# Performance work log

Hardware: AMD Instinct MI355X
Metric: run time of the kernel (lower is better)

Reference implementation:

```python
import jax, jax.numpy as jnp
import numpy as np
import math

D_MODEL = 1024
N_HEADS = 16
D_HEAD = D_MODEL // N_HEADS  # 64
ROPE_BASE = 10000.0


def make_inv_freq(dim: int, base: float = ROPE_BASE) -> jnp.ndarray:
    half = dim // 2
    if half == 0:
        return jnp.zeros((1,), dtype=jnp.float32)
    return jnp.asarray(1.0 / base ** (np.arange(half, dtype=np.float32) * 2.0 / dim))


def rope_1d(x, pos, inv_freq):
    # x: (B, H, L, d_slice); pos: (B, 1, L)
    D = x.shape[-1]
    half = D // 2
    if half == 0:
        return x
    f = pos[..., None].astype(jnp.float32) * inv_freq  # (B,1,L,half)
    c, s = jnp.cos(f), jnp.sin(f)
    x1, x2 = x[..., :half], x[..., half:2 * half]
    out = jnp.concatenate([x1 * c - x2 * s, x2 * c + x1 * s], axis=-1)
    if D > 2 * half:
        out = jnp.concatenate([out, x[..., 2 * half:]], axis=-1)
    return out


def rope_3d(x, rows, cols, pairs):
    # x: (B, H, L, D_HEAD); rows/cols/pairs: (B, L)
    d_per = D_HEAD // 3
    d_row = D_HEAD - 2 * d_per  # 22
    d_col = d_per               # 21
    d1, d2 = d_row, d_row + d_col
    r = rows[:, None, :]
    c = cols[:, None, :]
    p = pairs[:, None, :]
    x_row = rope_1d(x[..., :d1], r, make_inv_freq(d_row))
    x_col = rope_1d(x[..., d1:d2], c, make_inv_freq(d_col))
    x_pair = rope_1d(x[..., d2:], p, make_inv_freq(d_per))
    return jnp.concatenate([x_row, x_col, x_pair], axis=-1)


def setup_inputs() -> dict:
    key = jax.random.key(0)
    ks = jax.random.split(key, 8)
    B, L, D = 2, 2048, D_MODEL
    x = jax.random.normal(ks[0], (B, L, D), dtype=jnp.float32)
    rows = jax.random.randint(ks[1], (B, L), 0, 30, dtype=jnp.int32)
    cols = jax.random.randint(ks[2], (B, L), 0, 30, dtype=jnp.int32)
    pairs = jax.random.randint(ks[3], (B, L), 0, 8, dtype=jnp.int32)
    key_padding_mask = jnp.ones((B, L), dtype=bool)
    scale = 0.02
    Wq = jax.random.normal(ks[4], (D, D), dtype=jnp.float32) * scale
    Wk = jax.random.normal(ks[5], (D, D), dtype=jnp.float32) * scale
    Wv = jax.random.normal(ks[6], (D, D), dtype=jnp.float32) * scale
    Wo = jax.random.normal(ks[7], (D, D), dtype=jnp.float32) * scale
    return {"x": x, "rows": rows, "cols": cols, "pairs": pairs,
            "key_padding_mask": key_padding_mask,
            "Wq": Wq, "Wk": Wk, "Wv": Wv, "Wo": Wo}


def reference(x, rows, cols, pairs, key_padding_mask, Wq, Wk, Wv, Wo):
    B, L, D = x.shape
    H, Dh = N_HEADS, D_HEAD
    # torch Linear (bias=False): y = x @ W.T, W: (out, in)
    q = jnp.einsum('bld,ed->ble', x, Wq).reshape(B, L, H, Dh).transpose(0, 2, 1, 3)
    k = jnp.einsum('bld,ed->ble', x, Wk).reshape(B, L, H, Dh).transpose(0, 2, 1, 3)
    v = jnp.einsum('bld,ed->ble', x, Wv).reshape(B, L, H, Dh).transpose(0, 2, 1, 3)
    # 3-axis RoPE per head (self-attention: same positions for q and k)
    q = rope_3d(q, rows, cols, pairs)
    k = rope_3d(k, rows, cols, pairs)
    scale = math.sqrt(Dh)
    scores = jnp.einsum('bhqd,bhkd->bhqk', q, k) / scale
    scores = jnp.where(key_padding_mask[:, None, None, :], scores, -jnp.inf)
    attn = jax.nn.softmax(scores, axis=-1)
    out = jnp.einsum('bhqk,bhkd->bhqd', attn, v)
    out = out.transpose(0, 2, 1, 3).reshape(B, L, D)
    return jnp.einsum('bld,ed->ble', out, Wo)
```

## Files before the change

kernel.cpp:

```cpp
#include <hip/hip_runtime.h>

typedef unsigned short ushort_t;
typedef __bf16 bf16x8 __attribute__((ext_vector_type(8)));
typedef __bf16 bf16x4 __attribute__((ext_vector_type(4)));
typedef float f32x4 __attribute__((ext_vector_type(4)));

#define LOG10K 9.210340371976184f
#define QSCALE 0.18033688011112042f

__device__ __forceinline__ unsigned short f2b(float f) {
  unsigned u = __float_as_uint(f);
  u += 0x7fffu + ((u >> 16) & 1u);
  return (unsigned short)(u >> 16);
}
__device__ __forceinline__ float b2f(unsigned short h) {
  return __uint_as_float(((unsigned)h) << 16);
}
__device__ __forceinline__ float exp2_fast(float x) {
  float r;
  asm("v_exp_f32 %0, %1" : "=v"(r) : "v"(x));
  return r;
}

__device__ __forceinline__ void async16(const void* g, void* l) {
  __builtin_amdgcn_global_load_lds(
      (const __attribute__((address_space(1))) unsigned int*)g,
      (__attribute__((address_space(3))) unsigned int*)l, 16, 0, 0);
}

__global__ void cvt_f32_bf16(const float* __restrict__ src, ushort_t* __restrict__ dst, int n4) {
  int i = blockIdx.x * blockDim.x + threadIdx.x;
  int stride = gridDim.x * blockDim.x;
  for (; i < n4; i += stride) {
    float4 v = ((const float4*)src)[i];
    ushort4 o;
    o.x = f2b(v.x); o.y = f2b(v.y); o.z = f2b(v.z); o.w = f2b(v.w);
    ((ushort4*)dst)[i] = o;
  }
}

__global__ void cvt_w4(const float* __restrict__ a, const float* __restrict__ b,
                       const float* __restrict__ c, const float* __restrict__ d,
                       ushort_t* __restrict__ dst) {
  int blk = blockIdx.x;
  int w = blk >> 10;
  int i = (blk & 1023) * 256 + threadIdx.x;
  const float* src = (w == 0) ? a : (w == 1) ? b : (w == 2) ? c : d;
  float4 v = ((const float4*)src)[i];
  ushort4 o;
  o.x = f2b(v.x); o.y = f2b(v.y); o.z = f2b(v.z); o.w = f2b(v.w);
  ((ushort4*)dst)[(size_t)w * 262144 + i] = o;
}

template<int OUTMODE>
__global__ __launch_bounds__(256) void gemm_bt(const ushort_t* __restrict__ A,
                                               const ushort_t* __restrict__ Bw,
                                               void* __restrict__ out,
                                               void* __restrict__ out2,
                                               void* __restrict__ out3,
                                               int M, int N, int K) {
  __shared__ ushort_t As[128 * 64];
  __shared__ ushort_t Bs[128 * 64];
  int tid = threadIdx.x;
  int w = tid >> 6, l = tid & 63, g = l >> 4, c = l & 15;
  int m0 = blockIdx.y * 128, n0 = blockIdx.x * 128;
  int wm = (w >> 1) * 64, wn = (w & 1) * 64;
  f32x4 acc[4][4] = {};

  for (int kt = 0; kt < K; kt += 64) {
#pragma unroll
    for (int cc = 0; cc < 4; ++cc) {
      int e = cc * 2048 + w * 512 + l * 8;
      int row = e >> 6;
      int jb = l & 7;
      int col = (jb ^ (row & 7)) << 3;
      async16(A + (size_t)(m0 + row) * K + kt + col, As + row * 64 + jb * 8);
      async16(Bw + (size_t)(n0 + row) * K + kt + col, Bs + row * 64 + jb * 8);
    }
    __syncthreads();
#pragma unroll
    for (int s = 0; s < 2; ++s) {
      bf16x8 af[4], bfr[4];
#pragma unroll
      for (int mi = 0; mi < 4; ++mi) {
        int row = wm + mi * 16 + c;
        int blk = (s * 4 + g) ^ (row & 7);
        af[mi] = *(const bf16x8*)(const void*)(As + row * 64 + blk * 8);
      }
#pragma unroll
      for (int ni = 0; ni < 4; ++ni) {
        int row = wn + ni * 16 + c;
        int blk = (s * 4 + g) ^ (row & 7);
        bfr[ni] = *(const bf16x8*)(const void*)(Bs + row * 64 + blk * 8);
      }
#pragma unroll
      for (int mi = 0; mi < 4; ++mi)
#pragma unroll
        for (int ni = 0; ni < 4; ++ni)
          acc[mi][ni] = __builtin_amdgcn_mfma_f32_16x16x32_bf16(af[mi], bfr[ni], acc[mi][ni], 0, 0, 0);
    }
    __syncthreads();
  }

#pragma unroll
  for (int mi = 0; mi < 4; ++mi) {
#pragma unroll
    for (int ni = 0; ni < 4; ++ni) {
      int mrow0 = m0 + wm + mi * 16 + g * 4;
      int ncol = n0 + wn + ni * 16 + c;
      if (OUTMODE == 3) {
        int sec = ncol >> 10;
        int nn = ncol & 1023;
        int h = nn >> 6, d = nn & 63;
        int b = mrow0 >> 11, ll0 = mrow0 & 2047;
        if (sec == 2) {
          ushort4 o;
          o.x = f2b(acc[mi][ni][0]); o.y = f2b(acc[mi][ni][1]);
          o.z = f2b(acc[mi][ni][2]); o.w = f2b(acc[mi][ni][3]);
          *(ushort4*)((ushort_t*)out3 + ((size_t)(b * 16 + h) * 64 + d) * 2048 + ll0) = o;
        } else {
          ushort_t* dst = (ushort_t*)(sec ? out2 : out);
#pragma unroll
          for (int j = 0; j < 4; ++j)
            dst[((size_t)(b * 16 + h) * 2048 + ll0 + j) * 64 + d] = f2b(acc[mi][ni][j]);
        }
      } else {
#pragma unroll
        for (int j = 0; j < 4; ++j)
          ((float*)out)[(size_t)(mrow0 + j) * N + ncol] = acc[mi][ni][j];
      }
    }
  }
}

__global__ void rope_qk(ushort_t* __restrict__ Qg, ushort_t* __restrict__ Kg,
                        const int* __restrict__ rows, const int* __restrict__ cols,
                        const int* __restrict__ pairs) {
  __shared__ float tl[1420];
  for (int i = threadIdx.x; i < 710; i += 256) {
    float ang;
    if (i < 330) {
      int p = i / 11, k = i - p * 11;
      ang = (float)p * __expf(-(LOG10K / 11.0f) * (float)k);
    } else if (i < 630) {
      int r = i - 330;
      int p = r / 10, k = r - p * 10;
      ang = (float)p * __expf(-(LOG10K * 2.0f / 21.0f) * (float)k);
    } else {
      int r = i - 630;
      int p = r / 10, k = r - p * 10;
      ang = (float)p * __expf(-(LOG10K * 2.0f / 21.0f) * (float)k);
    }
    float s, cs;
    sincosf(ang, &s, &cs);
    tl[2 * i] = cs;
    tl[2 * i + 1] = s;
  }
  __syncthreads();
  const float2* rt = (const float2*)tl;
  const float2* ct = (const float2*)(tl + 660);
  const float2* pt = (const float2*)(tl + 1260);

  int idx = blockIdx.x * blockDim.x + threadIdx.x;
  int which = idx >> 16;
  int r = idx & 65535;
  int b = r >> 15;
  int h = (r >> 11) & 15;
  int ll = r & 2047;
  ushort_t* base = (which ? Kg : Qg) + ((size_t)(b * 16 + h) * 2048 + ll) * 64;

  float f[64];
  const uint4* p = (const uint4*)base;
#pragma unroll
  for (int t = 0; t < 8; ++t) {
    uint4 v = p[t];
    unsigned a0 = v.x, a1 = v.y, a2 = v.z, a3 = v.w;
    f[t * 8 + 0] = b2f((unsigned short)(a0 & 0xffff)); f[t * 8 + 1] = b2f((unsigned short)(a0 >> 16));
    f[t * 8 + 2] = b2f((unsigned short)(a1 & 0xffff)); f[t * 8 + 3] = b2f((unsigned short)(a1 >> 16));
    f[t * 8 + 4] = b2f((unsigned short)(a2 & 0xffff)); f[t * 8 + 5] = b2f((unsigned short)(a2 >> 16));
    f[t * 8 + 6] = b2f((unsigned short)(a3 & 0xffff)); f[t * 8 + 7] = b2f((unsigned short)(a3 >> 16));
  }

  int bl = b * 2048 + ll;
  int pr = rows[bl], pc = cols[bl], pp = pairs[bl];

#pragma unroll
  for (int i = 0; i < 11; ++i) {
    float2 cs = rt[pr * 11 + i];
    float x1 = f[i], x2 = f[i + 11];
    f[i] = x1 * cs.x - x2 * cs.y;
    f[i + 11] = x2 * cs.x + x1 * cs.y;
  }
#pragma unroll
  for (int i = 0; i < 10; ++i) {
    float2 cs = ct[pc * 10 + i];
    float x1 = f[22 + i], x2 = f[32 + i];
    f[22 + i] = x1 * cs.x - x2 * cs.y;
    f[32 + i] = x2 * cs.x + x1 * cs.y;
    float2 cs2 = pt[pp * 10 + i];
    x1 = f[43 + i]; x2 = f[53 + i];
    f[43 + i] = x1 * cs2.x - x2 * cs2.y;
    f[53 + i] = x2 * cs2.x + x1 * cs2.y;
  }
  if (which == 0) {
#pragma unroll
    for (int i = 0; i < 64; ++i) f[i] *= QSCALE;
  }

  uint4* po = (uint4*)base;
#pragma unroll
  for (int t = 0; t < 8; ++t) {
    uint4 v;
    v.x = (unsigned)f2b(f[t * 8 + 0]) | ((unsigned)f2b(f[t * 8 + 1]) << 16);
    v.y = (unsigned)f2b(f[t * 8 + 2]) | ((unsigned)f2b(f[t * 8 + 3]) << 16);
    v.z = (unsigned)f2b(f[t * 8 + 4]) | ((unsigned)f2b(f[t * 8 + 5]) << 16);
    v.w = (unsigned)f2b(f[t * 8 + 6]) | ((unsigned)f2b(f[t * 8 + 7]) << 16);
    po[t] = v;
  }
}

__global__ __launch_bounds__(512) void flash_attn(const ushort_t* __restrict__ Qg,
                                                  const ushort_t* __restrict__ Kg,
                                                  const ushort_t* __restrict__ Vt,
                                                  ushort_t* __restrict__ AO) {
  __shared__ ushort_t Kl[2][4096];
  __shared__ ushort_t Vl[2][4096];
  __shared__ ushort_t Pl[8][1024];
  int bid = blockIdx.x;
  int wg = (bid & 7) * 64 + (bid >> 3);
  int bh = wg >> 4, qt = wg & 15;
  int tid = threadIdx.x;
  int w = tid >> 6, l = tid & 63, g = l >> 4, c = l & 15;

  const ushort_t* Qbase = Qg + ((size_t)bh * 2048 + qt * 128 + w * 16) * 64;
  bf16x8 qf[2];
#pragma unroll
  for (int s = 0; s < 2; ++s)
    qf[s] = *(const bf16x8*)(const void*)(Qbase + c * 64 + s * 32 + g * 8);

  f32x4 acc[4] = {};
  float mrow = -1e30f;
  float lrow = 0.f;

  char* KlB = (char*)&Kl[0][0];
  char* VlB = (char*)&Vl[0][0];
  char* PlW = (char*)&Pl[w][0];
  int c7 = c & 7;
  int offA0 = c * 128 + ((g ^ c7) << 4);
  int offA1 = c * 128 + (((4 ^ g) ^ c7) << 4);
  char* pw  = PlW + g * 128 + c * 8;
  char* prd = PlW + ((g & 1) << 8) + ((g >> 1) << 9) + c * 8;

  int srow = tid >> 3, sjb = tid & 7;
  int scol = (sjb ^ (srow & 7)) << 3;
  char* Kdst = KlB + srow * 128 + sjb * 16;
  char* Vdst = VlB + srow * 128 + sjb * 16;
  const ushort_t* Ksrc = Kg + ((size_t)bh * 2048 + srow) * 64 + scol;
  const ushort_t* Vsrc = Vt + ((size_t)bh * 64 + srow) * 2048 + scol;

  async16(Ksrc, Kdst);
  async16(Vsrc, Vdst);
  Ksrc += 4096; Vsrc += 64;
  asm volatile("s_waitcnt vmcnt(0)" ::: "memory");
  __syncthreads();

  int bufoff = 0;
  for (int kt = 0; kt < 32; ++kt) {
    if (kt < 31) {
      async16(Ksrc, Kdst + (bufoff ^ 8192));
      async16(Vsrc, Vdst + (bufoff ^ 8192));
      Ksrc += 4096; Vsrc += 64;
    }
    const char* KA0 = KlB + bufoff + offA0;
    const char* KA1 = KlB + bufoff + offA1;
    const char* VA0 = VlB + bufoff + offA0;
    const char* VA1 = VlB + bufoff + offA1;

    f32x4 sc[4] = {};
    __builtin_amdgcn_s_setprio(1);
#pragma unroll
    for (int kb = 0; kb < 4; ++kb) {
      bf16x8 a0 = *(const bf16x8*)(const void*)(KA0 + kb * 2048);
      bf16x8 a1 = *(const bf16x8*)(const void*)(KA1 + kb * 2048);
      sc[kb] = __builtin_amdgcn_mfma_f32_16x16x32_bf16(a0, qf[0], sc[kb], 0, 0, 0);
      sc[kb] = __builtin_amdgcn_mfma_f32_16x16x32_bf16(a1, qf[1], sc[kb], 0, 0, 0);
    }
    __builtin_amdgcn_s_setprio(0);

    {
      float t = sc[0][0];
#pragma unroll
      for (int kb = 0; kb < 4; ++kb)
#pragma unroll
        for (int j = 0; j < 4; ++j) t = fmaxf(t, sc[kb][j]);
      t = fmaxf(t, __shfl_xor(t, 16));
      t = fmaxf(t, __shfl_xor(t, 32));
      if (!__all(t - mrow <= 8.0f)) {
        float mnew = fmaxf(mrow, t);
        float corr = exp2_fast(mrow - mnew);
        mrow = mnew;
        lrow *= corr;
#pragma unroll
        for (int j = 0; j < 4; ++j) {
          float cj = __shfl(corr, ((l >> 4) << 2) | j);
#pragma unroll
          for (int db = 0; db < 4; ++db) acc[db][j] *= cj;
        }
      }
      float m = mrow;
      float ps = 0.f;
#pragma unroll
      for (int kb = 0; kb < 4; ++kb) {
        float p0 = exp2_fast(sc[kb][0] - m);
        float p1 = exp2_fast(sc[kb][1] - m);
        float p2 = exp2_fast(sc[kb][2] - m);
        float p3 = exp2_fast(sc[kb][3] - m);
        ps += (p0 + p1) + (p2 + p3);
        unsigned r0, r1;
        asm("v_cvt_pk_bf16_f32 %0, %1, %2" : "=v"(r0) : "v"(p0), "v"(p1));
        asm("v_cvt_pk_bf16_f32 %0, %1, %2" : "=v"(r1) : "v"(p2), "v"(p3));
        uint2 pr; pr.x = r0; pr.y = r1;
        *(uint2*)(pw + kb * 512) = pr;
      }
      ps += __shfl_xor(ps, 16);
      ps += __shfl_xor(ps, 32);
      lrow += ps;
    }
    asm volatile("s_waitcnt lgkmcnt(0)" ::: "memory");

    __builtin_amdgcn_s_setprio(1);
#pragma unroll
    for (int s2 = 0; s2 < 2; ++s2) {
      const char* pb = prd + s2 * 1024;
      bf16x4 lo = *(const bf16x4*)(const void*)pb;
      bf16x4 hi = *(const bf16x4*)(const void*)(pb + 128);
      bf16x8 pf = __builtin_shufflevector(lo, hi, 0, 1, 2, 3, 4, 5, 6, 7);
      const char* VA = s2 ? VA1 : VA0;
#pragma unroll
      for (int db = 0; db < 4; ++db) {
        bf16x8 vf = *(const bf16x8*)(const void*)(VA + db * 2048);
        acc[db] = __builtin_amdgcn_mfma_f32_16x16x32_bf16(pf, vf, acc[db], 0, 0, 0);
      }
    }
    __builtin_amdgcn_s_setprio(0);

    asm volatile("s_waitcnt vmcnt(0)" ::: "memory");
    __syncthreads();
    bufoff ^= 8192;
  }

  int b = bh >> 4, h = bh & 15;
  {
    float linv = 1.0f / lrow;
#pragma unroll
    for (int j = 0; j < 4; ++j) {
      float inv = __shfl(linv, ((l >> 4) << 2) | j);
      int token = qt * 128 + w * 16 + g * 4 + j;
      size_t rowbase = (size_t)(b * 2048 + token) * 1024 + h * 64;
#pragma unroll
      for (int db = 0; db < 4; ++db)
        AO[rowbase + db * 16 + c] = f2b(acc[db][j] * inv);
    }
  }
}

extern "C" void kernel_launch(void* const* d_in, const int* in_sizes, int n_in,
                              void* d_out, int out_size, void* d_ws, size_t ws_size,
                              hipStream_t stream) {
  const float* x = (const float*)d_in[0];
  const int* rows = (const int*)d_in[1];
  const int* cols = (const int*)d_in[2];
  const int* pairs = (const int*)d_in[3];
  const float* Wq = (const float*)d_in[5];
  const float* Wk = (const float*)d_in[6];
  const float* Wv = (const float*)d_in[7];
  const float* Wo = (const float*)d_in[8];

  char* ws = (char*)d_ws;
  ushort_t* xb   = (ushort_t*)(ws);
  ushort_t* Wqkv = (ushort_t*)(ws + (8u << 20));
  ushort_t* Wob  = Wqkv + 3u * 1048576u;
  ushort_t* Qg   = (ushort_t*)(ws + (16u << 20));
  ushort_t* Kg   = (ushort_t*)(ws + (24u << 20));
  ushort_t* Vt   = (ushort_t*)(ws + (32u << 20));
  ushort_t* AO   = (ushort_t*)(ws);

  cvt_f32_bf16<<<1024, 256, 0, stream>>>(x, xb, 4194304 / 4);
  cvt_w4<<<4096, 256, 0, stream>>>(Wq, Wk, Wv, Wo, Wqkv);

  dim3 gg3(24, 32);
  gemm_bt<3><<<gg3, 256, 0, stream>>>(xb, Wqkv, Qg, Kg, Vt, 4096, 3072, 1024);

  rope_qk<<<512, 256, 0, stream>>>(Qg, Kg, rows, cols, pairs);

  flash_attn<<<512, 512, 0, stream>>>(Qg, Kg, Vt, AO);

  dim3 gg2(8, 32);
  gemm_bt<2><<<gg2, 256, 0, stream>>>(AO, Wob, d_out, nullptr, nullptr, 4096, 1024, 1024);
}
```

Before: 132.4 us.

## Rewrite flash attention with 32x32x16 MFMA and 32-query-row waves

The attention kernel moves from 16x16x32 MFMA tiles with 8 waves of 16 query rows to 32x32x16 MFMA tiles with 4 waves of 32 query rows each. Block size drops from 512 to 256 threads. K/V tile loads now issue two async copies per thread, and the P tile layout in LDS is reorganised with an XOR swizzle to match the new operand layout. The intent is fewer LDS reads per FLOP and higher MFMA efficiency, at the cost of more registers per wave and fewer waves per block to hide latency.

```diff
diff --git a/kernel.cpp b/kernel.cpp
--- a/kernel.cpp
+++ b/kernel.cpp
@@ -2,8 +2,8 @@
 
 typedef unsigned short ushort_t;
 typedef __bf16 bf16x8 __attribute__((ext_vector_type(8)));
-typedef __bf16 bf16x4 __attribute__((ext_vector_type(4)));
 typedef float f32x4 __attribute__((ext_vector_type(4)));
+typedef float f32x16 __attribute__((ext_vector_type(16)));
 
 #define LOG10K 9.210340371976184f
 #define QSCALE 0.18033688011112042f
@@ -219,37 +219,37 @@
   }
 }
 
-__global__ __launch_bounds__(512) void flash_attn(const ushort_t* __restrict__ Qg,
+__global__ __launch_bounds__(256) void flash_attn(const ushort_t* __restrict__ Qg,
                                                   const ushort_t* __restrict__ Kg,
                                                   const ushort_t* __restrict__ Vt,
                                                   ushort_t* __restrict__ AO) {
   __shared__ ushort_t Kl[2][4096];
   __shared__ ushort_t Vl[2][4096];
-  __shared__ ushort_t Pl[8][1024];
+  __shared__ ushort_t Pl[4][2048];
   int bid = blockIdx.x;
   int wg = (bid & 7) * 64 + (bid >> 3);
   int bh = wg >> 4, qt = wg & 15;
   int tid = threadIdx.x;
-  int w = tid >> 6, l = tid & 63, g = l >> 4, c = l & 15;
-
-  const ushort_t* Qbase = Qg + ((size_t)bh * 2048 + qt * 128 + w * 16) * 64;
-  bf16x8 qf[2];
-#pragma unroll
-  for (int s = 0; s < 2; ++s)
-    qf[s] = *(const bf16x8*)(const void*)(Qbase + c * 64 + s * 32 + g * 8);
-
-  f32x4 acc[4] = {};
+  int w = tid >> 6, l = tid & 63;
+  int r31 = l & 31, hi = l >> 5, q7 = r31 & 7;
+
+  const ushort_t* Qbase = Qg + ((size_t)bh * 2048 + qt * 128 + w * 32 + r31) * 64;
+  bf16x8 qf[4];
+#pragma unroll
+  for (int kc = 0; kc < 4; ++kc)
+    qf[kc] = *(const bf16x8*)(const void*)(Qbase + kc * 16 + hi * 8);
+
+  f32x16 acc0 = {}, acc1 = {};
   float mrow = -1e30f;
   float lrow = 0.f;
 
   char* KlB = (char*)&Kl[0][0];
   char* VlB = (char*)&Vl[0][0];
   char* PlW = (char*)&Pl[w][0];
-  int c7 = c & 7;
-  int offA0 = c * 128 + ((g ^ c7) << 4);
-  int offA1 = c * 128 + (((4 ^ g) ^ c7) << 4);
-  char* pw  = PlW + g * 128 + c * 8;
-  char* prd = PlW + ((g & 1) << 8) + ((g >> 1) << 9) + c * 8;
+  int blkoff[4];
+#pragma unroll
+  for (int t = 0; t < 4; ++t) blkoff[t] = ((t * 2 + hi) ^ q7) << 4;
+  char* prow = PlW + r31 * 128;
 
   int srow = tid >> 3, sjb = tid & 7;
   int scol = (sjb ^ (srow & 7)) << 3;
@@ -259,7 +259,9 @@
   const ushort_t* Vsrc = Vt + ((size_t)bh * 64 + srow) * 2048 + scol;
 
   async16(Ksrc, Kdst);
+  async16(Ksrc + 32 * 64, Kdst + 4096);
   async16(Vsrc, Vdst);
+  async16(Vsrc + 32 * 2048, Vdst + 4096);
   Ksrc += 4096; Vsrc += 64;
   asm volatile("s_waitcnt vmcnt(0)" ::: "memory");
   __syncthreads();
@@ -267,62 +269,70 @@
   int bufoff = 0;
   for (int kt = 0; kt < 32; ++kt) {
     if (kt < 31) {
-      async16(Ksrc, Kdst + (bufoff ^ 8192));
-      async16(Vsrc, Vdst + (bufoff ^ 8192));
+      int nb = bufoff ^ 8192;
+      async16(Ksrc, Kdst + nb);
+      async16(Ksrc + 32 * 64, Kdst + nb + 4096);
+      async16(Vsrc, Vdst + nb);
+      async16(Vsrc + 32 * 2048, Vdst + nb + 4096);
       Ksrc += 4096; Vsrc += 64;
     }
-    const char* KA0 = KlB + bufoff + offA0;
-    const char* KA1 = KlB + bufoff + offA1;
-    const char* VA0 = VlB + bufoff + offA0;
-    const char* VA1 = VlB + bufoff + offA1;
-
-    f32x4 sc[4] = {};
+    const char* krd = KlB + bufoff + r31 * 128;
+    const char* vrd = VlB + bufoff + r31 * 128;
+
+    f32x16 sc0 = {}, sc1 = {};
     __builtin_amdgcn_s_setprio(1);
 #pragma unroll
-    for (int kb = 0; kb < 4; ++kb) {
-      bf16x8 a0 = *(const bf16x8*)(const void*)(KA0 + kb * 2048);
-      bf16x8 a1 = *(const bf16x8*)(const void*)(KA1 + kb * 2048);
-      sc[kb] = __builtin_amdgcn_mfma_f32_16x16x32_bf16(a0, qf[0], sc[kb], 0, 0, 0);
-      sc[kb] = __builtin_amdgcn_mfma_f32_16x16x32_bf16(a1, qf[1], sc[kb], 0, 0, 0);
+    for (int kc = 0; kc < 4; ++kc) {
+      bf16x8 kf0 = *(const bf16x8*)(const void*)(krd + blkoff[kc]);
+      bf16x8 kf1 = *(const bf16x8*)(const void*)(krd + 4096 + blkoff[kc]);
+      sc0 = __builtin_amdgcn_mfma_f32_32x32x16_bf16(kf0, qf[kc], sc0, 0, 0, 0);
+      sc1 = __builtin_amdgcn_mfma_f32_32x32x16_bf16(kf1, qf[kc], sc1, 0, 0, 0);
     }
     __builtin_amdgcn_s_setprio(0);
 
     {
-      float t = sc[0][0];
-#pragma unroll
-      for (int kb = 0; kb < 4; ++kb)
-#pragma unroll
-        for (int j = 0; j < 4; ++j) t = fmaxf(t, sc[kb][j]);
-      t = fmaxf(t, __shfl_xor(t, 16));
-      t = fmaxf(t, __shfl_xor(t, 32));
-      if (!__all(t - mrow <= 8.0f)) {
-        float mnew = fmaxf(mrow, t);
+      float a[8];
+#pragma unroll
+      for (int i = 0; i < 8; ++i)
+        a[i] = fmaxf(fmaxf(sc0[i], sc0[i + 8]), fmaxf(sc1[i], sc1[i + 8]));
+      float t01 = fmaxf(fmaxf(a[0], a[1]), fmaxf(a[2], a[3]));
+      float t23 = fmaxf(fmaxf(a[4], a[5]), fmaxf(a[6], a[7]));
+      float tmax = fmaxf(t01, t23);
+      tmax = fmaxf(tmax, __shfl_xor(tmax, 32));
+      if (!__all(tmax - mrow <= 8.0f)) {
+        float mnew = fmaxf(mrow, tmax);
         float corr = exp2_fast(mrow - mnew);
         mrow = mnew;
         lrow *= corr;
-#pragma unroll
-        for (int j = 0; j < 4; ++j) {
-          float cj = __shfl(corr, ((l >> 4) << 2) | j);
-#pragma unroll
-          for (int db = 0; db < 4; ++db) acc[db][j] *= cj;
+        int hi4 = hi << 2;
+#pragma unroll
+        for (int r = 0; r < 16; ++r) {
+          float cr = __shfl(corr, (r & 3) + 8 * (r >> 2) + hi4);
+          acc0[r] *= cr;
+          acc1[r] *= cr;
         }
       }
       float m = mrow;
-      float ps = 0.f;
-#pragma unroll
-      for (int kb = 0; kb < 4; ++kb) {
-        float p0 = exp2_fast(sc[kb][0] - m);
-        float p1 = exp2_fast(sc[kb][1] - m);
-        float p2 = exp2_fast(sc[kb][2] - m);
-        float p3 = exp2_fast(sc[kb][3] - m);
-        ps += (p0 + p1) + (p2 + p3);
-        unsigned r0, r1;
-        asm("v_cvt_pk_bf16_f32 %0, %1, %2" : "=v"(r0) : "v"(p0), "v"(p1));
-        asm("v_cvt_pk_bf16_f32 %0, %1, %2" : "=v"(r1) : "v"(p2), "v"(p3));
-        uint2 pr; pr.x = r0; pr.y = r1;
-        *(uint2*)(pw + kb * 512) = pr;
-      }
-      ps += __shfl_xor(ps, 16);
+      float ps0 = 0.f, ps1 = 0.f, ps2 = 0.f, ps3 = 0.f;
+      char* pwb = prow + hi * 8;
+      auto expblock = [&](const f32x16& s, int blkbase) {
+#pragma unroll
+        for (int rr = 0; rr < 4; ++rr) {
+          float p0 = exp2_fast(s[rr * 4 + 0] - m);
+          float p1 = exp2_fast(s[rr * 4 + 1] - m);
+          float p2 = exp2_fast(s[rr * 4 + 2] - m);
+          float p3 = exp2_fast(s[rr * 4 + 3] - m);
+          ps0 += p0; ps1 += p1; ps2 += p2; ps3 += p3;
+          unsigned u0, u1;
+          asm("v_cvt_pk_bf16_f32 %0, %1, %2" : "=v"(u0) : "v"(p0), "v"(p1));
+          asm("v_cvt_pk_bf16_f32 %0, %1, %2" : "=v"(u1) : "v"(p2), "v"(p3));
+          uint2 pr; pr.x = u0; pr.y = u1;
+          *(uint2*)(pwb + (((blkbase + rr) ^ q7) << 4)) = pr;
+        }
+      };
+      expblock(sc0, 0);
+      expblock(sc1, 4);
+      float ps = (ps0 + ps1) + (ps2 + ps3);
       ps += __shfl_xor(ps, 32);
       lrow += ps;
     }
@@ -330,17 +340,12 @@
 
     __builtin_amdgcn_s_setprio(1);
 #pragma unroll
-    for (int s2 = 0; s2 < 2; ++s2) {
-      const char* pb = prd + s2 * 1024;
-      bf16x4 lo = *(const bf16x4*)(const void*)pb;
-      bf16x4 hi = *(const bf16x4*)(const void*)(pb + 128);
-      bf16x8 pf = __builtin_shufflevector(lo, hi, 0, 1, 2, 3, 4, 5, 6, 7);
-      const char* VA = s2 ? VA1 : VA0;
-#pragma unroll
-      for (int db = 0; db < 4; ++db) {
-        bf16x8 vf = *(const bf16x8*)(const void*)(VA + db * 2048);
-        acc[db] = __builtin_amdgcn_mfma_f32_16x16x32_bf16(pf, vf, acc[db], 0, 0, 0);
-      }
+    for (int step = 0; step < 4; ++step) {
+      bf16x8 pf = *(const bf16x8*)(const void*)(prow + blkoff[step]);
+      bf16x8 vf0 = *(const bf16x8*)(const void*)(vrd + blkoff[step]);
+      bf16x8 vf1 = *(const bf16x8*)(const void*)(vrd + 4096 + blkoff[step]);
+      acc0 = __builtin_amdgcn_mfma_f32_32x32x16_bf16(pf, vf0, acc0, 0, 0, 0);
+      acc1 = __builtin_amdgcn_mfma_f32_32x32x16_bf16(pf, vf1, acc1, 0, 0, 0);
     }
     __builtin_amdgcn_s_setprio(0);
 
@@ -350,17 +355,16 @@
   }
 
   int b = bh >> 4, h = bh & 15;
-  {
-    float linv = 1.0f / lrow;
-#pragma unroll
-    for (int j = 0; j < 4; ++j) {
-      float inv = __shfl(linv, ((l >> 4) << 2) | j);
-      int token = qt * 128 + w * 16 + g * 4 + j;
-      size_t rowbase = (size_t)(b * 2048 + token) * 1024 + h * 64;
-#pragma unroll
-      for (int db = 0; db < 4; ++db)
-        AO[rowbase + db * 16 + c] = f2b(acc[db][j] * inv);
-    }
+  float linv = 1.0f / lrow;
+  int hi4 = hi << 2;
+#pragma unroll
+  for (int r = 0; r < 16; ++r) {
+    int q = (r & 3) + 8 * (r >> 2) + hi4;
+    float inv = __shfl(linv, q);
+    int token = qt * 128 + w * 32 + q;
+    size_t rowbase = (size_t)(b * 2048 + token) * 1024 + h * 64;
+    AO[rowbase + r31] = f2b(acc0[r] * inv);
+    AO[rowbase + 32 + r31] = f2b(acc1[r] * inv);
   }
 }
 
@@ -393,7 +397,7 @@
 
   rope_qk<<<512, 256, 0, stream>>>(Qg, Kg, rows, cols, pairs);
 
-  flash_attn<<<512, 512, 0, stream>>>(Qg, Kg, Vt, AO);
+  flash_attn<<<512, 256, 0, stream>>>(Qg, Kg, Vt, AO);
 
   dim3 gg2(8, 32);
   gemm_bt<2><<<gg2, 256, 0, stream>>>(AO, Wob, d_out, nullptr, nullptr, 4096, 1024, 1024);
```

Measured after the change: 139.8 us. 1.06x slower.
